# Performance work log

Measured on AMD Instinct MI355X. Metric: run time of the kernel, lower is better.

## Reference

```python
import jax, jax.numpy as jnp
import numpy as np

B, DIM, N = 64, 128, 4000
H = 4
DH = DIM // H          # 32
CL = 50                # clusters (hardcoded in module)
K = 9                  # knn_num
SCALOR = DH ** -0.5


def setup_inputs() -> dict:
    key = jax.random.key(0)
    ks = jax.random.split(key, 16)
    s = 0.05
    inp = {
        'x': jax.random.normal(ks[0], (B, DIM, N, 1), jnp.float32),
        # conv_group1 / conv_group2: InstanceNorm(no affine) -> BN(affine) -> ReLU -> 1x1 conv
        'wg1': jax.random.normal(ks[1], (CL, DIM), jnp.float32) * s,
        'bg1': jnp.zeros((CL,), jnp.float32),
        'g1_gamma': jnp.ones((DIM,), jnp.float32),
        'g1_beta': jnp.zeros((DIM,), jnp.float32),
        'wg2': jax.random.normal(ks[2], (CL, DIM), jnp.float32) * s,
        'bg2': jnp.zeros((CL,), jnp.float32),
        'g2_gamma': jnp.ones((DIM,), jnp.float32),
        'g2_beta': jnp.zeros((DIM,), jnp.float32),
        # per-head 1x1 convs (stacked over heads)
        'qkv_w': jax.random.normal(ks[3], (H, DH, DIM), jnp.float32) * s,
        'qkv_b': jnp.zeros((H, DH), jnp.float32),
        'qkv1_w': jax.random.normal(ks[4], (H, 3 * DH, DIM), jnp.float32) * s,
        'qkv1_b': jnp.zeros((H, 3 * DH), jnp.float32),
        # GCBlock convs: conv1 (1,3) stride (1,3): 2*DH->DH ; conv2 (1,3): DH->DH
        'gc1_w': jax.random.normal(ks[5], (H, DH, 2 * DH, 3), jnp.float32) * s,
        'gc1_b': jnp.zeros((H, DH), jnp.float32),
        'gc1_gamma': jnp.ones((H, DH), jnp.float32),
        'gc1_beta': jnp.zeros((H, DH), jnp.float32),
        'gc2_w': jax.random.normal(ks[6], (H, DH, DH, 3), jnp.float32) * s,
        'gc2_b': jnp.zeros((H, DH), jnp.float32),
        'gc2_gamma': jnp.ones((H, DH), jnp.float32),
        'gc2_beta': jnp.zeros((H, DH), jnp.float32),
        # output projections
        'pres_w': jax.random.normal(ks[7], (DIM, 2 * DIM), jnp.float32) * s,
        'pres_b': jnp.zeros((DIM,), jnp.float32),
        'proj_w': jax.random.normal(ks[8], (DIM, DIM), jnp.float32) * s,
        'proj_b': jnp.zeros((DIM,), jnp.float32),
    }
    return inp


def _conv_group(x3, w, bconv, gamma, beta):
    # x3: (b, C, n). InstanceNorm2d(eps=1e-3, no affine) over n, BN(train) over (b,n), ReLU, 1x1 conv.
    mu = x3.mean(-1, keepdims=True)
    var = x3.var(-1, keepdims=True)
    xin = (x3 - mu) * jax.lax.rsqrt(var + 1e-3)
    mu2 = xin.mean((0, 2), keepdims=True)
    var2 = xin.var((0, 2), keepdims=True)
    xbn = gamma[None, :, None] * (xin - mu2) * jax.lax.rsqrt(var2 + 1e-5) + beta[None, :, None]
    xr = jax.nn.relu(xbn)
    return jnp.einsum('oc,bcn->bon', w, xr) + bconv[None, :, None]


def _bn_train(h, gamma, beta, axes):
    mu = h.mean(axes, keepdims=True)
    var = h.var(axes, keepdims=True)
    return gamma * (h - mu) * jax.lax.rsqrt(var + 1e-5) + beta


def _forward(x, wg1, bg1, g1_gamma, g1_beta, wg2, bg2, g2_gamma, g2_beta,
             qkv_w, qkv_b, qkv1_w, qkv1_b,
             gc1_w, gc1_b, gc1_gamma, gc1_beta,
             gc2_w, gc2_b, gc2_gamma, gc2_beta,
             pres_w, pres_b, proj_w, proj_b):
    xs = x[..., 0]                                          # (b, dim, n)
    # cluster assignment 1: softmax over points
    embed1 = _conv_group(xs, wg1, bg1, g1_gamma, g1_beta)   # (b, 50, n)
    S1 = jax.nn.softmax(embed1, axis=2)
    cluster_x = jnp.einsum('bdn,bcn->bdc', xs, S1)          # (b, dim, 50)

    # ---- local branch (per head, vectorized): 1x1 conv -> knn graph feature -> conv stack ----
    q = jnp.einsum('hod,bdc->bhoc', qkv_w, cluster_x) + qkv_b[None, :, :, None]  # (b,H,dh,50)
    xt = q.transpose(0, 1, 3, 2)                            # (b,H,50,dh)
    inner = jnp.einsum('bhnc,bhmc->bhnm', xt, xt)
    sq = jnp.sum(xt * xt, axis=-1)
    pd = 2.0 * inner - sq[..., :, None] - sq[..., None, :]  # negative squared distance
    idx = jax.lax.top_k(pd, K)[1]                            # (b,H,50,K)
    x_exp = jnp.broadcast_to(xt[:, :, None, :, :], xt.shape[:2] + (CL, CL, DH))
    feature = jnp.take_along_axis(x_exp, idx[..., None], axis=3)        # (b,H,50,K,dh)
    center = jnp.broadcast_to(xt[:, :, :, None, :], feature.shape)
    edge = jnp.concatenate([center, center - feature], axis=-1)          # (b,H,50,K,2dh)
    # conv1: kernel (1,3) stride (1,3): K=9 -> 3 windows of 3
    e = edge.reshape(edge.shape[0], H, CL, 3, 3, 2 * DH)
    h1 = jnp.einsum('bhnjti,hoit->bhnjo', e, gc1_w) + gc1_b[None, :, None, None, :]
    h1 = jax.nn.relu(_bn_train(h1, gc1_gamma[None, :, None, None, :], gc1_beta[None, :, None, None, :], (0, 2, 3)))
    # conv2: kernel (1,3): 3 -> 1
    h2 = jnp.einsum('bhnti,hoit->bhno', h1, gc2_w) + gc2_b[None, :, None, :]
    h2 = jax.nn.relu(_bn_train(h2, gc2_gamma[None, :, None, :], gc2_beta[None, :, None, :], (0, 2)))
    local = h2.transpose(0, 1, 3, 2)                        # (b,H,dh,50)

    # ---- global branch: tiny attention over 50 clusters per head ----
    qkv = jnp.einsum('hod,bdc->bhoc', qkv1_w, cluster_x) + qkv1_b[None, :, :, None]  # (b,H,3dh,50)
    qg, kg, vg = jnp.split(qkv, 3, axis=2)
    attn = jax.nn.softmax(SCALOR * jnp.einsum('bhdn,bhdm->bhnm', qg, kg), axis=-1)
    glob = jnp.einsum('bhnm,bhdm->bhdn', attn, vg)          # (b,H,dh,50)

    # interleave [local_h, global_h] per head along channels -> (b, 2*dim, 50)
    per_head = jnp.concatenate([local, glob], axis=2)       # (b,H,2dh,50)
    cat = per_head.reshape(per_head.shape[0], 2 * DIM, CL)
    res = jnp.einsum('oc,bcn->bon', pres_w, cat) + pres_b[None, :, None]  # (b,dim,50)

    # cluster assignment 2: softmax over clusters, scatter back to points
    embed2 = _conv_group(xs, wg2, bg2, g2_gamma, g2_beta)   # (b,50,n)
    S2 = jax.nn.softmax(embed2, axis=1)
    res2 = jnp.einsum('bdc,bcn->bdn', res, S2)              # (b,dim,n)
    out = jnp.einsum('od,bdn->bon', proj_w, res2) + proj_b[None, :, None]
    return out[..., None]                                   # (b,dim,n,1)


def reference(x, wg1, bg1, g1_gamma, g1_beta, wg2, bg2, g2_gamma, g2_beta,
              qkv_w, qkv_b, qkv1_w, qkv1_b,
              gc1_w, gc1_b, gc1_gamma, gc1_beta,
              gc2_w, gc2_b, gc2_gamma, gc2_beta,
              pres_w, pres_b, proj_w, proj_b):
    return _forward(x, wg1, bg1, g1_gamma, g1_beta, wg2, bg2, g2_gamma, g2_beta,
                    qkv_w, qkv_b, qkv1_w, qkv1_b,
                    gc1_w, gc1_b, gc1_gamma, gc1_beta,
                    gc2_w, gc2_b, gc2_gamma, gc2_beta,
                    pres_w, pres_b, proj_w, proj_b)
```

## Files before the change

### kernel.cpp

```cpp
#include <hip/hip_runtime.h>
#include <cstddef>


constexpr size_t O_MU    = 0;
constexpr size_t O_RINV  = 8192;
constexpr size_t O_RATIO = 16384;
constexpr size_t O_A1    = 24576;
constexpr size_t O_B1    = 24704;
constexpr size_t O_A2    = 24832;
constexpr size_t O_B2    = 24960;
constexpr size_t O_PROJWT= 25088;
constexpr size_t O_VPROJ = 41472;
constexpr size_t O_MT    = 41600;
constexpr size_t O_E2    = 74368;
constexpr size_t O_UCXP  = 12874368;
constexpr size_t O_XT    = 17068672;
constexpr size_t O_QT    = 17478272;
constexpr size_t O_KT    = 17887872;
constexpr size_t O_VT    = 18297472;
constexpr size_t O_H1    = 18707072;
constexpr size_t O_P1    = 19935872;
constexpr size_t O_H2    = 19952512;
constexpr size_t O_P2    = 20362112;
constexpr size_t O_CAT   = 20378752;
constexpr size_t O_PRES2 = 21197952;

__global__ __launch_bounds__(256) void k_rowstats(const float* __restrict__ x,
                                                  float* __restrict__ ws){
  int w = threadIdx.x >> 6, lane = threadIdx.x & 63;
  int row = blockIdx.x*4 + w;
  const float4* xr = (const float4*)(x + (size_t)row * 4000);
  float s = 0.f, sq = 0.f;
  for(int i = lane; i < 1000; i += 64){
    float4 v = xr[i];
    s  += v.x + v.y + v.z + v.w;
    sq += v.x*v.x + v.y*v.y + v.z*v.z + v.w*v.w;
  }
  for(int off = 32; off > 0; off >>= 1){
    s  += __shfl_down(s,  off, 64);
    sq += __shfl_down(sq, off, 64);
  }
  if(lane == 0){
    float mean = s * (1.f/4000.f);
    float var  = sq * (1.f/4000.f) - mean*mean;
    ws[O_MU   + row] = mean;
    ws[O_RINV + row] = rsqrtf(var + 1e-3f);
    ws[O_RATIO+ row] = var / (var + 1e-3f);
  }
}

__global__ __launch_bounds__(256) void k_prep(const float* g1g, const float* g1b,
                       const float* g2g, const float* g2b,
                       const float* projw, float* __restrict__ ws){
  int t = threadIdx.x;
  int i = blockIdx.x*256 + t;
  { int o = i & 127, k = i >> 7; ws[O_PROJWT+i] = projw[o*128 + k]; }
  if(blockIdx.x == 0 && t < 128){
    float s = 0.f;
    for(int b = 0; b < 64; b++) s += ws[O_RATIO + b*128 + t];
    float var2 = s * (1.f/64.f);
    float inv2 = rsqrtf(var2 + 1e-5f);
    ws[O_A1+t] = g1g[t] * inv2;  ws[O_B1+t] = g1b[t];
    ws[O_A2+t] = g2g[t] * inv2;  ws[O_B2+t] = g2b[t];
  }
}

__global__ __launch_bounds__(256) void k_mprep(const float* __restrict__ presw,
                                               const float* __restrict__ presb,
                                               float* __restrict__ ws){
  int t = threadIdx.x;
  if(blockIdx.x < 128){
    int kk2 = blockIdx.x * 2;
    __shared__ float pwc[2][128];
    { int which = t >> 7, d = t & 127; pwc[which][d] = presw[d*256 + kk2 + which]; }
    __syncthreads();
    int which = t >> 7, o = t & 127;
    float acc = 0.f;
    for(int d = 0; d < 128; d++) acc += ws[O_PROJWT + d*128 + o] * pwc[which][d];
    ws[O_MT + (size_t)(kk2 + which)*128 + o] = acc;
  }else{
    if(t < 128){
      float v = 0.f;
      for(int d = 0; d < 128; d++) v += ws[O_PROJWT + d*128 + t] * presb[d];
      ws[O_VPROJ + t] = v;
    }
  }
}

__global__ __launch_bounds__(256) void k_e1ucx(const float* __restrict__ x,
    const float* __restrict__ wg1, const float* __restrict__ bg1,
    float* __restrict__ ws){
  int ch = blockIdx.x, b = blockIdx.y;
  __shared__ float lW1[128*52];
  __shared__ float lrv1[128*48];
  __shared__ float lxt [48*132];
  __shared__ float ca1[128], cb1[128];
  __shared__ float bg1p[56];
  int t = threadIdx.x;
  if(t < 128){
    float mu = ws[O_MU + b*128 + t], ri = ws[O_RINV + b*128 + t];
    float a1 = ws[O_A1+t]*ri;
    ca1[t] = a1; cb1[t] = ws[O_B1+t] - a1*mu;
  }
  if(t < 56) bg1p[t] = (t < 50) ? bg1[t] : 0.f;
  for(int i = t; i < 1664; i += 256){
    int cl = i >> 5, cq = i & 31;
    float4 w = (cl < 50) ? *(const float4*)&wg1[cl*128 + cq*4] : make_float4(0.f,0.f,0.f,0.f);
    int c0 = cq*4;
    lW1[(c0+0)*52+cl] = w.x; lW1[(c0+1)*52+cl] = w.y;
    lW1[(c0+2)*52+cl] = w.z; lW1[(c0+3)*52+cl] = w.w;
  }
  int dg = t & 31, cg = t >> 5;
  float ua[4][8];
  #pragma unroll
  for(int r = 0; r < 4; r++)
    #pragma unroll
    for(int i = 0; i < 8; i++) ua[r][i] = 0.f;
  float zacc = 0.f;
  int ig = t >> 4, jg = t & 15;
  int clb = ig*4, j4 = jg*4;
  int sc[6], sj[6];
  float4 pf[6];
  #pragma unroll
  for(int j = 0; j < 6; j++){ int i = t + 256*j; sc[j] = i/12; sj[j] = (i%12)*4; }
  #pragma unroll
  for(int j = 0; j < 6; j++)
    pf[j] = *(const float4*)&x[(size_t)(b*128 + sc[j])*4000 + ch*500 + sj[j]];

  for(int st = 0; st < 11; st++){
    int lim = (st == 10) ? 20 : 48;
    __syncthreads();
    #pragma unroll
    for(int j = 0; j < 6; j++){
      int c = sc[j], jj = sj[j];
      float4 xv = (jj < lim) ? pf[j] : make_float4(0.f,0.f,0.f,0.f);
      lxt[(jj+0)*132 + c] = xv.x; lxt[(jj+1)*132 + c] = xv.y;
      lxt[(jj+2)*132 + c] = xv.z; lxt[(jj+3)*132 + c] = xv.w;
      float a1 = ca1[c], b1v = cb1[c];
      float4 r1;
      r1.x = fmaxf(a1*xv.x + b1v, 0.f); r1.y = fmaxf(a1*xv.y + b1v, 0.f);
      r1.z = fmaxf(a1*xv.z + b1v, 0.f); r1.w = fmaxf(a1*xv.w + b1v, 0.f);
      *(float4*)&lrv1[c*48 + jj] = r1;
    }
    __syncthreads();
    if(st < 10){
      int lim2 = (st == 9) ? 20 : 48;
      int nb2 = ch*500 + (st+1)*48;
      #pragma unroll
      for(int j = 0; j < 6; j++)
        pf[j] = (sj[j] < lim2) ? *(const float4*)&x[(size_t)(b*128 + sc[j])*4000 + nb2 + sj[j]]
                               : make_float4(0.f,0.f,0.f,0.f);
    }
    float e[4][4];
    if(ig < 13 && jg < 12){
      #pragma unroll
      for(int r = 0; r < 4; r++){ e[r][0]=0.f; e[r][1]=0.f; e[r][2]=0.f; e[r][3]=0.f; }
      #pragma unroll 4
      for(int c = 0; c < 128; c++){
        float4 w = *(const float4*)&lW1[c*52 + clb];
        float4 v = *(const float4*)&lrv1[c*48 + j4];
        e[0][0] += w.x*v.x; e[0][1] += w.x*v.y; e[0][2] += w.x*v.z; e[0][3] += w.x*v.w;
        e[1][0] += w.y*v.x; e[1][1] += w.y*v.y; e[1][2] += w.y*v.z; e[1][3] += w.y*v.w;
        e[2][0] += w.z*v.x; e[2][1] += w.z*v.y; e[2][2] += w.z*v.z; e[2][3] += w.z*v.w;
        e[3][0] += w.w*v.x; e[3][1] += w.w*v.y; e[3][2] += w.w*v.z; e[3][3] += w.w*v.w;
      }
    }
    __syncthreads();
    if(ig < 13 && jg < 12){
      bool live = (j4 < lim);
      #pragma unroll
      for(int r = 0; r < 4; r++){
        float bias = bg1p[clb + r];
        float4 u = make_float4(0.f,0.f,0.f,0.f);
        if(live){
          u.x = expf(e[r][0] + bias); u.y = expf(e[r][1] + bias);
          u.z = expf(e[r][2] + bias); u.w = expf(e[r][3] + bias);
        }
        *(float4*)&lrv1[(clb + r)*48 + j4] = u;
      }
    }
    __syncthreads();
    if(t < 224){
      int d4 = dg*4, c8 = cg*8;
      for(int n4 = 0; n4 < 12; n4++){
        int n0 = n4*4;
        float4 uv[8];
        #pragma unroll
        for(int i = 0; i < 8; i++) uv[i] = *(const float4*)&lrv1[(c8 + i)*48 + n0];
        {
          float4 xq = *(const float4*)&lxt[(n0+0)*132 + d4];
          #pragma unroll
          for(int i = 0; i < 8; i++){
            float u = uv[i].x;
            ua[0][i] += xq.x*u; ua[1][i] += xq.y*u; ua[2][i] += xq.z*u; ua[3][i] += xq.w*u;
          }
        }
        {
          float4 xq = *(const float4*)&lxt[(n0+1)*132 + d4];
          #pragma unroll
          for(int i = 0; i < 8; i++){
            float u = uv[i].y;
            ua[0][i] += xq.x*u; ua[1][i] += xq.y*u; ua[2][i] += xq.z*u; ua[3][i] += xq.w*u;
          }
        }
        {
          float4 xq = *(const float4*)&lxt[(n0+2)*132 + d4];
          #pragma unroll
          for(int i = 0; i < 8; i++){
            float u = uv[i].z;
            ua[0][i] += xq.x*u; ua[1][i] += xq.y*u; ua[2][i] += xq.z*u; ua[3][i] += xq.w*u;
          }
        }
        {
          float4 xq = *(const float4*)&lxt[(n0+3)*132 + d4];
          #pragma unroll
          for(int i = 0; i < 8; i++){
            float u = uv[i].w;
            ua[0][i] += xq.x*u; ua[1][i] += xq.y*u; ua[2][i] += xq.z*u; ua[3][i] += xq.w*u;
          }
        }
      }
    }
    if(t < 52){
      float s = 0.f;
      #pragma unroll
      for(int k = 0; k < 12; k++){
        float4 u = *(const float4*)&lrv1[t*48 + k*4];
        s += u.x + u.y + u.z + u.w;
      }
      zacc += s;
    }
  }
  if(t < 224){
    int d4 = dg*4, c8 = cg*8;
    #pragma unroll
    for(int r = 0; r < 4; r++){
      size_t base = O_UCXP + ((size_t)(ch*64 + b)*132 + d4 + r)*56 + c8;
      *(float4*)&ws[base]     = make_float4(ua[r][0], ua[r][1], ua[r][2], ua[r][3]);
      *(float4*)&ws[base + 4] = make_float4(ua[r][4], ua[r][5], ua[r][6], ua[r][7]);
    }
  }
  if(t < 52) ws[O_UCXP + ((size_t)(ch*64 + b)*132 + 128)*56 + t] = zacc;
}

__global__ __launch_bounds__(256) void k_e2(const float* __restrict__ x,
    const float* __restrict__ wg2, const float* __restrict__ bg2,
    float* __restrict__ ws){
  int ch = blockIdx.x, b = blockIdx.y;
  __shared__ float lW2[128*52];
  __shared__ float lrv2[128*48];
  __shared__ float ca2[128], cb2[128];
  __shared__ float bg2p[56];
  int t = threadIdx.x;
  if(t < 128){
    float mu = ws[O_MU + b*128 + t], ri = ws[O_RINV + b*128 + t];
    float a2 = ws[O_A2+t]*ri;
    ca2[t] = a2; cb2[t] = ws[O_B2+t] - a2*mu;
  }
  if(t < 56) bg2p[t] = (t < 50) ? bg2[t] : 0.f;
  for(int i = t; i < 1664; i += 256){
    int cl = i >> 5, cq = i & 31;
    float4 w = (cl < 50) ? *(const float4*)&wg2[cl*128 + cq*4] : make_float4(0.f,0.f,0.f,0.f);
    int c0 = cq*4;
    lW2[(c0+0)*52+cl] = w.x; lW2[(c0+1)*52+cl] = w.y;
    lW2[(c0+2)*52+cl] = w.z; lW2[(c0+3)*52+cl] = w.w;
  }
  int ig = t >> 4, jg = t & 15;
  int clb = ig*4, j4 = jg*4;
  int sc[6], sj[6];
  float4 pf[6];
  #pragma unroll
  for(int j = 0; j < 6; j++){ int i = t + 256*j; sc[j] = i/12; sj[j] = (i%12)*4; }
  #pragma unroll
  for(int j = 0; j < 6; j++)
    pf[j] = *(const float4*)&x[(size_t)(b*128 + sc[j])*4000 + ch*500 + sj[j]];

  for(int st = 0; st < 11; st++){
    int nb = ch*500 + st*48;
    int lim = (st == 10) ? 20 : 48;
    __syncthreads();
    #pragma unroll
    for(int j = 0; j < 6; j++){
      int c = sc[j], jj = sj[j];
      float4 xv = (jj < lim) ? pf[j] : make_float4(0.f,0.f,0.f,0.f);
      float a2 = ca2[c], b2v = cb2[c];
      float4 r2;
      r2.x = fmaxf(a2*xv.x + b2v, 0.f); r2.y = fmaxf(a2*xv.y + b2v, 0.f);
      r2.z = fmaxf(a2*xv.z + b2v, 0.f); r2.w = fmaxf(a2*xv.w + b2v, 0.f);
      *(float4*)&lrv2[c*48 + jj] = r2;
    }
    __syncthreads();
    if(st < 10){
      int lim2 = (st == 9) ? 20 : 48;
      int nb2 = ch*500 + (st+1)*48;
      #pragma unroll
      for(int j = 0; j < 6; j++)
        pf[j] = (sj[j] < lim2) ? *(const float4*)&x[(size_t)(b*128 + sc[j])*4000 + nb2 + sj[j]]
                               : make_float4(0.f,0.f,0.f,0.f);
    }
    if(ig < 13 && jg < 12){
      float e[4][4];
      #pragma unroll
      for(int r = 0; r < 4; r++){ e[r][0]=0.f; e[r][1]=0.f; e[r][2]=0.f; e[r][3]=0.f; }
      #pragma unroll 4
      for(int c = 0; c < 128; c++){
        float4 w = *(const float4*)&lW2[c*52 + clb];
        float4 v = *(const float4*)&lrv2[c*48 + j4];
        e[0][0] += w.x*v.x; e[0][1] += w.x*v.y; e[0][2] += w.x*v.z; e[0][3] += w.x*v.w;
        e[1][0] += w.y*v.x; e[1][1] += w.y*v.y; e[1][2] += w.y*v.z; e[1][3] += w.y*v.w;
        e[2][0] += w.z*v.x; e[2][1] += w.z*v.y; e[2][2] += w.z*v.z; e[2][3] += w.z*v.w;
        e[3][0] += w.w*v.x; e[3][1] += w.w*v.y; e[3][2] += w.w*v.z; e[3][3] += w.w*v.w;
      }
      if(j4 < lim){
        #pragma unroll
        for(int r = 0; r < 4; r++){
          int cl = clb + r;
          if(cl < 50){
            float bias = bg2p[cl];
            float4 o = make_float4(e[r][0]+bias, e[r][1]+bias, e[r][2]+bias, e[r][3]+bias);
            *(float4*)&ws[O_E2 + ((size_t)b*50 + cl)*4000 + nb + j4] = o;
          }
        }
      }
    }
  }
}

__global__ __launch_bounds__(256) void k_qkv(const float* __restrict__ qw,
                                             const float* __restrict__ qb,
                                             const float* __restrict__ q1w,
                                             const float* __restrict__ q1b,
                                             float* __restrict__ ws){
  int rt = blockIdx.x, b = blockIdx.y;
  __shared__ float wl[64*130];
  __shared__ float cxl[128*52];
  __shared__ float zi[52];
  int t = threadIdx.x;
  if(t < 52){
    float s = 0.f;
    if(t < 50){
      #pragma unroll
      for(int ch = 0; ch < 8; ch++)
        s += ws[O_UCXP + ((size_t)(ch*64 + b)*132 + 128)*56 + t];
      zi[t] = 1.f / s;
    }else zi[t] = 0.f;
  }
  for(int i = t; i < 2048; i += 256){
    int rl = i >> 5, kq = i & 31, row = rt*64 + rl;
    float4 w = (row < 128) ? *(const float4*)&qw[row*128 + kq*4]
                           : *(const float4*)&q1w[(row-128)*128 + kq*4];
    int k0 = kq*4;
    wl[rl*130 + k0+0] = w.x; wl[rl*130 + k0+1] = w.y;
    wl[rl*130 + k0+2] = w.z; wl[rl*130 + k0+3] = w.w;
  }
  __syncthreads();
  for(int i = t; i < 6656; i += 256){
    int k = i / 52, c = i % 52;
    float s = 0.f;
    size_t base = O_UCXP + ((size_t)b*132 + k)*56 + c;
    #pragma unroll
    for(int ch = 0; ch < 8; ch++) s += ws[base + (size_t)ch*64*132*56];
    cxl[i] = s * zi[c];
  }
  __syncthreads();
  int ig = t & 15, cg = t >> 4;
  float acc[4][4];
  #pragma unroll
  for(int r = 0; r < 4; r++){ acc[r][0]=0.f; acc[r][1]=0.f; acc[r][2]=0.f; acc[r][3]=0.f; }
// ... 24 lines not shown
      }
      #pragma unroll
      for(int s = 0; s < 4; s++){
        int c = cg*4 + s;
        if(c < 50) ws[base + (size_t)c*32] = acc[r][s] + bias;
      }
    }
  }
}

__global__ __launch_bounds__(256) void k_knn(const float* __restrict__ g1w,
                                             const float* __restrict__ g1bias,
                                             float* __restrict__ ws){
  int h = blockIdx.x, b = blockIdx.y;
  __shared__ float xtl[50][33];
  __shared__ float pdl[50][52];
  __shared__ float sql[50];
  __shared__ int   idxl[50][9];
  __shared__ float w1l[6144];
  int t = threadIdx.x;
  const float* xtg = ws + O_XT + (size_t)(b*4 + h)*1600;
  for(int i = t; i < 1600; i += 256) xtl[i >> 5][i & 31] = xtg[i];
  for(int i = t; i < 6144; i += 256){
    int o = i / 192, r = i % 192, ii = r / 3, tt = r % 3;
    w1l[(ii*3 + tt)*32 + o] = g1w[(size_t)h*6144 + i];
  }
  __syncthreads();
  if(t < 50){
    float s = 0.f;
    for(int d = 0; d < 32; d++){ float v = xtl[t][d]; s += v*v; }
    sql[t] = s;
  }
  __syncthreads();
  for(int i = t; i < 2500; i += 256){
    int n = i / 50, m = i % 50;
    float s = 0.f;
    for(int d = 0; d < 32; d++) s += xtl[n][d]*xtl[m][d];
    pdl[n][m] = 2.f*s - sql[n] - sql[m];
  }
  __syncthreads();
  if(t < 50){
    float pv = INFINITY; int pi = -1;
    for(int k = 0; k < 9; k++){
      float bv = -INFINITY; int bi = 1000;
      for(int m = 0; m < 50; m++){
        float v = pdl[t][m];
        bool elig = (v < pv) || (v == pv && m > pi);
        if(elig && (v > bv || (v == bv && m < bi))){ bv = v; bi = m; }
      }
      idxl[t][k] = bi; pv = bv; pi = bi;
    }
  }
  __syncthreads();
  if(t < 150){
    int n = t / 3, jw = t % 3;
    float acc[32];
    #pragma unroll
    for(int o = 0; o < 32; o++) acc[o] = 0.f;
    for(int t3 = 0; t3 < 3; t3++){
      int kx = idxl[n][jw*3 + t3];
      for(int ii = 0; ii < 32; ii++){
        float c0 = xtl[n][ii];
        float c1 = c0 - xtl[kx][ii];
        const float* wr0 = w1l + (ii*3 + t3)*32;
        const float* wr1 = w1l + ((ii+32)*3 + t3)*32;
        #pragma unroll
        for(int o = 0; o < 32; o++) acc[o] += c0*wr0[o] + c1*wr1[o];
      }
    }
    float* out = ws + O_H1 + ((size_t)(b*4 + h)*150 + n*3 + jw)*32;
    #pragma unroll
    for(int o = 0; o < 32; o++) out[o] = acc[o] + g1bias[h*32 + o];
  }
}

__global__ __launch_bounds__(256) void k_bn1p(float* __restrict__ ws){
  int h = blockIdx.x, b = blockIdx.y, t = threadIdx.x;
  int o = t & 31, part = t >> 5;
  const float* src = ws + O_H1 + (size_t)(b*4 + h)*4800;
  float s = 0.f, sq = 0.f;
  for(int nj = part; nj < 150; nj += 8){
    float v = src[nj*32 + o];
    s += v; sq += v*v;
  }
  __shared__ float rs[8][33], rq[8][33];
  rs[part][o] = s; rq[part][o] = sq; __syncthreads();
  if(t < 32){
    float S = 0.f, Q = 0.f;
    for(int p = 0; p < 8; p++){ S += rs[p][t]; Q += rq[p][t]; }
    ws[O_P1 + b*256 + h*32 + t]       = S;
    ws[O_P1 + b*256 + 128 + h*32 + t] = Q;
  }
}

__global__ __launch_bounds__(256) void k_conv2(const float* __restrict__ g1g,
                                               const float* __restrict__ g1be,
                                               const float* __restrict__ g2w,
                                               const float* __restrict__ g2bias,
                                               float* __restrict__ ws){
  int h = blockIdx.x, b = blockIdx.y;
  __shared__ float hl[150][33];
  __shared__ float w2l[3072];
  __shared__ float rs[8][32], rq[8][32];
  __shared__ float b1s[32], b1t[32];
  int t = threadIdx.x;
  if(t < 32){
    float s = 0.f, sq = 0.f;
    for(int bb = 0; bb < 64; bb++){
      s  += ws[O_P1 + bb*256 + h*32 + t];
      sq += ws[O_P1 + bb*256 + 128 + h*32 + t];
    }
    float mean = s * (1.f/9600.f), var = sq * (1.f/9600.f) - mean*mean;
    float sc = g1g[h*32+t] * rsqrtf(var + 1e-5f);
    b1s[t] = sc; b1t[t] = g1be[h*32+t] - sc*mean;
  }
  for(int i = t; i < 3072; i += 256){
    int o = i / 96, r = i % 96, ii = r / 3, tt = r % 3;
    w2l[(ii*3 + tt)*32 + o] = g2w[(size_t)h*3072 + i];
  }
  __syncthreads();
  const float* h1p = ws + O_H1 + (size_t)(b*4 + h)*4800;
  for(int i = t; i < 4800; i += 256){
    int nj = i >> 5, ii = i & 31;
    hl[nj][ii] = fmaxf(b1s[ii]*h1p[i] + b1t[ii], 0.f);
  }
  __syncthreads();
  int o = t & 31, ng = t >> 5;
  float bias = g2bias[h*32 + o];
  float s = 0.f, sq = 0.f;
  for(int n = ng; n < 50; n += 8){
    float acc = 0.f;
    for(int t3 = 0; t3 < 3; t3++){
      const float* hr = hl[n*3 + t3];
      #pragma unroll
      for(int ii = 0; ii < 32; ii++) acc += hr[ii] * w2l[(ii*3 + t3)*32 + o];
    }
    acc += bias;
    ws[O_H2 + ((size_t)(b*4 + h)*50 + n)*32 + o] = acc;
    s += acc; sq += acc*acc;
  }
  rs[ng][o] = s; rq[ng][o] = sq; __syncthreads();
  if(t < 32){
    float S = 0.f, Q = 0.f;
    for(int g2 = 0; g2 < 8; g2++){ S += rs[g2][t]; Q += rq[g2][t]; }
// ... 4 lines not shown

__global__ __launch_bounds__(256) void k_attn(const float* __restrict__ g2g,
                                              const float* __restrict__ g2be,
                                              float* __restrict__ ws){
  int h = blockIdx.x, b = blockIdx.y;
  __shared__ float qtl[50][33], ktl[50][33], vtl[50][33], al[50][52];
  __shared__ float b2s[32], b2t[32];
  int t = threadIdx.x;
  if(t < 32){
    float s = 0.f, sq = 0.f;
    for(int bb = 0; bb < 64; bb++){
      s  += ws[O_P2 + (size_t)(bb*4 + h)*64 + t];
      sq += ws[O_P2 + (size_t)(bb*4 + h)*64 + 32 + t];
    }
    float mean = s * (1.f/3200.f), var = sq * (1.f/3200.f) - mean*mean;
    float sc = g2g[h*32+t] * rsqrtf(var + 1e-5f);
    b2s[t] = sc; b2t[t] = g2be[h*32+t] - sc*mean;
  }
  size_t base = (size_t)(b*4 + h)*1600;
  for(int i = t; i < 1600; i += 256){
    int n = i >> 5, d = i & 31;
    qtl[n][d] = ws[O_QT + base + i];
    ktl[n][d] = ws[O_KT + base + i];
    vtl[n][d] = ws[O_VT + base + i];
  }
  __syncthreads();
  for(int i = t; i < 2500; i += 256){
    int n = i / 50, m = i % 50;
    float s = 0.f;
    for(int d = 0; d < 32; d++) s += qtl[n][d]*ktl[m][d];
    al[n][m] = s * 0.17677669529663687f;
  }
  __syncthreads();
  if(t < 50){
    float m = -INFINITY;
    for(int j = 0; j < 50; j++) m = fmaxf(m, al[t][j]);
    float s = 0.f;
    for(int j = 0; j < 50; j++){ float e = expf(al[t][j] - m); al[t][j] = e; s += e; }
    float inv = 1.f/s;
    for(int j = 0; j < 50; j++) al[t][j] *= inv;
  }
  __syncthreads();
  for(int i = t; i < 1600; i += 256){
    int n = i >> 5, d = i & 31;
    float gacc = 0.f;
    for(int m = 0; m < 50; m++) gacc += al[n][m]*vtl[m][d];
    ws[O_CAT + ((size_t)b*256 + h*64 + 32 + d)*50 + n] = gacc;
    float l = fmaxf(b2s[d]*ws[O_H2 + ((size_t)(b*4 + h)*50 + n)*32 + d] + b2t[d], 0.f);
    ws[O_CAT + ((size_t)b*256 + h*64 + d)*50 + n] = l;
  }
}

__global__ __launch_bounds__(256) void k_res(float* __restrict__ ws){
  int b = blockIdx.x;
  __shared__ float mtl[64*132];
  __shared__ float catl[64*52];
  __shared__ float vp[128];
  int t = threadIdx.x;
  if(t < 128) vp[t] = ws[O_VPROJ + t];
  int og = t >> 4, cg = t & 15;
  int ob = og*8, cb = cg*4;
  float acc[8][4];
  #pragma unroll
  for(int r = 0; r < 8; r++){ acc[r][0]=0.f; acc[r][1]=0.f; acc[r][2]=0.f; acc[r][3]=0.f; }
  for(int kc = 0; kc < 4; kc++){
    int k0 = kc*64;
    __syncthreads();
    for(int i = t; i < 2048; i += 256){
      int k = i >> 5, oq = i & 31;
      float4 m = *(const float4*)&ws[O_MT + (size_t)(k0 + k)*128 + oq*4];
      *(float4*)&mtl[k*132 + oq*4] = m;
    }
    for(int i = t; i < 3328; i += 256){
      int k = i / 52, c = i % 52;
      catl[i] = (c < 50) ? ws[O_CAT + (size_t)b*12800 + (k0 + k)*50 + c] : 0.f;
    }
    __syncthreads();
    if(cg < 13){
      #pragma unroll 2
      for(int k = 0; k < 64; k++){
        float4 m0 = *(const float4*)&mtl[k*132 + ob];
        float4 m1 = *(const float4*)&mtl[k*132 + ob + 4];
        float4 cv = *(const float4*)&catl[k*52 + cb];
        acc[0][0] += m0.x*cv.x; acc[0][1] += m0.x*cv.y; acc[0][2] += m0.x*cv.z; acc[0][3] += m0.x*cv.w;
        acc[1][0] += m0.y*cv.x; acc[1][1] += m0.y*cv.y; acc[1][2] += m0.y*cv.z; acc[1][3] += m0.y*cv.w;
        acc[2][0] += m0.z*cv.x; acc[2][1] += m0.z*cv.y; acc[2][2] += m0.z*cv.z; acc[2][3] += m0.z*cv.w;
        acc[3][0] += m0.w*cv.x; acc[3][1] += m0.w*cv.y; acc[3][2] += m0.w*cv.z; acc[3][3] += m0.w*cv.w;
        acc[4][0] += m1.x*cv.x; acc[4][1] += m1.x*cv.y; acc[4][2] += m1.x*cv.z; acc[4][3] += m1.x*cv.w;
        acc[5][0] += m1.y*cv.x; acc[5][1] += m1.y*cv.y; acc[5][2] += m1.y*cv.z; acc[5][3] += m1.y*cv.w;
        acc[6][0] += m1.z*cv.x; acc[6][1] += m1.z*cv.y; acc[6][2] += m1.z*cv.z; acc[6][3] += m1.z*cv.w;
        acc[7][0] += m1.w*cv.x; acc[7][1] += m1.w*cv.y; acc[7][2] += m1.w*cv.z; acc[7][3] += m1.w*cv.w;
      }
    }
  }
  if(cg < 13){
    #pragma unroll
    for(int s = 0; s < 4; s++){
      int c = cb + s;
      if(c < 50){
        float4 o0 = make_float4(acc[0][s]+vp[ob+0], acc[1][s]+vp[ob+1], acc[2][s]+vp[ob+2], acc[3][s]+vp[ob+3]);
        float4 o1 = make_float4(acc[4][s]+vp[ob+4], acc[5][s]+vp[ob+5], acc[6][s]+vp[ob+6], acc[7][s]+vp[ob+7]);
        *(float4*)&ws[O_PRES2 + (size_t)b*6400 + c*128 + ob]     = o0;
        *(float4*)&ws[O_PRES2 + (size_t)b*6400 + c*128 + ob + 4] = o1;
      }
    }
  }
}

__global__ __launch_bounds__(256) void k_out(const float* __restrict__ projb,
                                             float* __restrict__ ws,
                                             float* __restrict__ out){
  int nt = blockIdx.x, b = blockIdx.y;
  int n0 = nt*64;
  __shared__ float sl[50*64];
  __shared__ float p2l[50*132];
  __shared__ float pb[128];
  int t = threadIdx.x;
  for(int i = t; i < 3200; i += 256){
    int c = i >> 6, j = i & 63, n = n0 + j;
    sl[i] = (n < 4000) ? ws[O_E2 + ((size_t)b*50 + c)*4000 + n] : 0.f;
  }
  for(int i = t; i < 6400; i += 256){
    int c = i >> 7, o = i & 127;
    p2l[c*132 + o] = ws[O_PRES2 + (size_t)b*6400 + c*128 + o];
  }
  if(t < 128) pb[t] = projb[t];
  __syncthreads();
  if(t < 64){
    int j = t;
    float m = -INFINITY;
    for(int c = 0; c < 50; c++) m = fmaxf(m, sl[c*64 + j]);
    float s = 0.f;
    for(int c = 0; c < 50; c++){ float e = expf(sl[c*64 + j] - m); sl[c*64 + j] = e; s += e; }
    float inv = 1.f/s;
    for(int c = 0; c < 50; c++) sl[c*64 + j] *= inv;
  }
  __syncthreads();
  int og = t >> 4, jg = t & 15;
  int ob = og*8, j4 = jg*4;
  float acc[8][4];
  #pragma unroll
  for(int r = 0; r < 8; r++){ acc[r][0]=0.f; acc[r][1]=0.f; acc[r][2]=0.f; acc[r][3]=0.f; }
  #pragma unroll 2
  for(int c = 0; c < 50; c++){
    float4 sv = *(const float4*)&sl[c*64 + j4];
    float4 p0 = *(const float4*)&p2l[c*132 + ob];
    float4 p1 = *(const float4*)&p2l[c*132 + ob + 4];
    acc[0][0] += p0.x*sv.x; acc[0][1] += p0.x*sv.y; acc[0][2] += p0.x*sv.z; acc[0][3] += p0.x*sv.w;
    acc[1][0] += p0.y*sv.x; acc[1][1] += p0.y*sv.y; acc[1][2] += p0.y*sv.z; acc[1][3] += p0.y*sv.w;
    acc[2][0] += p0.z*sv.x; acc[2][1] += p0.z*sv.y; acc[2][2] += p0.z*sv.z; acc[2][3] += p0.z*sv.w;
    acc[3][0] += p0.w*sv.x; acc[3][1] += p0.w*sv.y; acc[3][2] += p0.w*sv.z; acc[3][3] += p0.w*sv.w;
    acc[4][0] += p1.x*sv.x; acc[4][1] += p1.x*sv.y; acc[4][2] += p1.x*sv.z; acc[4][3] += p1.x*sv.w;
    acc[5][0] += p1.y*sv.x; acc[5][1] += p1.y*sv.y; acc[5][2] += p1.y*sv.z; acc[5][3] += p1.y*sv.w;
    acc[6][0] += p1.z*sv.x; acc[6][1] += p1.z*sv.y; acc[6][2] += p1.z*sv.z; acc[6][3] += p1.z*sv.w;
    acc[7][0] += p1.w*sv.x; acc[7][1] += p1.w*sv.y; acc[7][2] += p1.w*sv.z; acc[7][3] += p1.w*sv.w;
  }
  int n = n0 + j4;
  if(n < 4000){
    #pragma unroll
    for(int r = 0; r < 8; r++){
      float bv = pb[ob + r];
      float4 o = make_float4(acc[r][0]+bv, acc[r][1]+bv, acc[r][2]+bv, acc[r][3]+bv);
      *(float4*)&out[(size_t)(b*128 + ob + r)*4000 + n] = o;
    }
  }
}

extern "C" void kernel_launch(void* const* d_in, const int* in_sizes, int n_in,
                              void* d_out, int out_size, void* d_ws, size_t ws_size,
                              hipStream_t stream){
  (void)in_sizes; (void)n_in; (void)out_size; (void)ws_size;
  const float* x      = (const float*)d_in[0];
  const float* wg1    = (const float*)d_in[1];
  const float* bg1    = (const float*)d_in[2];
  const float* g1g    = (const float*)d_in[3];
  const float* g1b    = (const float*)d_in[4];
  const float* wg2    = (const float*)d_in[5];
  const float* bg2    = (const float*)d_in[6];
  const float* g2g    = (const float*)d_in[7];
  const float* g2b    = (const float*)d_in[8];
  const float* qkvw   = (const float*)d_in[9];
  const float* qkvb   = (const float*)d_in[10];
  const float* qkv1w  = (const float*)d_in[11];
  const float* qkv1b  = (const float*)d_in[12];
  const float* gc1w   = (const float*)d_in[13];
  const float* gc1bias= (const float*)d_in[14];
  const float* gc1g   = (const float*)d_in[15];
  const float* gc1be  = (const float*)d_in[16];
  const float* gc2w   = (const float*)d_in[17];
  const float* gc2bias= (const float*)d_in[18];
  const float* gc2g   = (const float*)d_in[19];
  const float* gc2be  = (const float*)d_in[20];
  const float* presw  = (const float*)d_in[21];
  const float* presb  = (const float*)d_in[22];
  const float* projw  = (const float*)d_in[23];
  const float* projb  = (const float*)d_in[24];
  float* ws = (float*)d_ws;
  float* out = (float*)d_out;

  k_rowstats<<<2048, 256, 0, stream>>>(x, ws);
  k_prep<<<64, 256, 0, stream>>>(g1g, g1b, g2g, g2b, projw, ws);
  k_mprep<<<129, 256, 0, stream>>>(presw, presb, ws);
  k_e1ucx<<<dim3(8, 64), 256, 0, stream>>>(x, wg1, bg1, ws);
  k_e2<<<dim3(8, 64), 256, 0, stream>>>(x, wg2, bg2, ws);
  k_qkv<<<dim3(8, 64), 256, 0, stream>>>(qkvw, qkvb, qkv1w, qkv1b, ws);
  k_knn<<<dim3(4, 64), 256, 0, stream>>>(gc1w, gc1bias, ws);
  k_bn1p<<<dim3(4, 64), 256, 0, stream>>>(ws);
  k_conv2<<<dim3(4, 64), 256, 0, stream>>>(gc1g, gc1be, gc2w, gc2bias, ws);
  k_attn<<<dim3(4, 64), 256, 0, stream>>>(gc2g, gc2be, ws);
  k_res<<<64, 256, 0, stream>>>(ws);
  k_out<<<dim3(63, 64), 256, 0, stream>>>(projb, ws, out);
}
```

Before: 779.3 us.

## Merge small kernels, double block size in e1/e2, split k_res work

Folds the prep work into the stats and mprep kernels and folds the BN1 partial sums into the knn kernel, cutting three launches. k_e1ucx and k_e2 move to 512-thread blocks with smaller per-thread tiles, and k_e2 uses a finer grid (12 chunks of 336 points). The lxt shared buffer gets an XOR swizzle in place of padding. k_res is split across two blocks per batch by output half so more CUs are used. The cost is more synchronisation per block and a heavier knn kernel, in exchange for more parallelism and fewer launches.

```diff
diff --git a/kernel.cpp b/kernel.cpp
--- a/kernel.cpp
+++ b/kernel.cpp
@@ -25,8 +25,15 @@
 constexpr size_t O_CAT   = 20378752;
 constexpr size_t O_PRES2 = 21197952;
 
-__global__ __launch_bounds__(256) void k_rowstats(const float* __restrict__ x,
-                                                  float* __restrict__ ws){
+__global__ __launch_bounds__(256) void k_stats(const float* __restrict__ x,
+                                               const float* __restrict__ projw,
+                                               float* __restrict__ ws){
+  if(blockIdx.x >= 2048){
+    int i = (blockIdx.x - 2048)*256 + threadIdx.x;
+    int o = i & 127, k = i >> 7;
+    ws[O_PROJWT + i] = projw[o*128 + k];
+    return;
+  }
   int w = threadIdx.x >> 6, lane = threadIdx.x & 63;
   int row = blockIdx.x*4 + w;
   const float4* xr = (const float4*)(x + (size_t)row * 4000);
@@ -49,24 +56,12 @@
   }
 }
 
-__global__ __launch_bounds__(256) void k_prep(const float* g1g, const float* g1b,
-                       const float* g2g, const float* g2b,
-                       const float* projw, float* __restrict__ ws){
-  int t = threadIdx.x;
-  int i = blockIdx.x*256 + t;
-  { int o = i & 127, k = i >> 7; ws[O_PROJWT+i] = projw[o*128 + k]; }
-  if(blockIdx.x == 0 && t < 128){
-    float s = 0.f;
-    for(int b = 0; b < 64; b++) s += ws[O_RATIO + b*128 + t];
-    float var2 = s * (1.f/64.f);
-    float inv2 = rsqrtf(var2 + 1e-5f);
-    ws[O_A1+t] = g1g[t] * inv2;  ws[O_B1+t] = g1b[t];
-    ws[O_A2+t] = g2g[t] * inv2;  ws[O_B2+t] = g2b[t];
-  }
-}
-
 __global__ __launch_bounds__(256) void k_mprep(const float* __restrict__ presw,
                                                const float* __restrict__ presb,
+                                               const float* __restrict__ g1g,
+                                               const float* __restrict__ g1b,
+                                               const float* __restrict__ g2g,
+                                               const float* __restrict__ g2b,
                                                float* __restrict__ ws){
   int t = threadIdx.x;
   if(blockIdx.x < 128){
@@ -78,22 +73,31 @@
     float acc = 0.f;
     for(int d = 0; d < 128; d++) acc += ws[O_PROJWT + d*128 + o] * pwc[which][d];
     ws[O_MT + (size_t)(kk2 + which)*128 + o] = acc;
-  }else{
+  }else if(blockIdx.x == 128){
     if(t < 128){
       float v = 0.f;
       for(int d = 0; d < 128; d++) v += ws[O_PROJWT + d*128 + t] * presb[d];
       ws[O_VPROJ + t] = v;
     }
-  }
-}
-
-__global__ __launch_bounds__(256) void k_e1ucx(const float* __restrict__ x,
+  }else{
+    if(t < 128){
+      float s = 0.f;
+      for(int b = 0; b < 64; b++) s += ws[O_RATIO + b*128 + t];
+      float var2 = s * (1.f/64.f);
+      float inv2 = rsqrtf(var2 + 1e-5f);
+      ws[O_A1+t] = g1g[t] * inv2;  ws[O_B1+t] = g1b[t];
+      ws[O_A2+t] = g2g[t] * inv2;  ws[O_B2+t] = g2b[t];
+    }
+  }
+}
+
+__global__ __launch_bounds__(512, 4) void k_e1ucx(const float* __restrict__ x,
     const float* __restrict__ wg1, const float* __restrict__ bg1,
     float* __restrict__ ws){
   int ch = blockIdx.x, b = blockIdx.y;
   __shared__ float lW1[128*52];
   __shared__ float lrv1[128*48];
-  __shared__ float lxt [48*132];
+  __shared__ float lxt [48*128];
   __shared__ float ca1[128], cb1[128];
   __shared__ float bg1p[56];
   int t = threadIdx.x;
@@ -102,8 +106,8 @@
     float a1 = ws[O_A1+t]*ri;
     ca1[t] = a1; cb1[t] = ws[O_B1+t] - a1*mu;
   }
-  if(t < 56) bg1p[t] = (t < 50) ? bg1[t] : 0.f;
-  for(int i = t; i < 1664; i += 256){
+  if(t >= 448 && t < 504){ int q = t - 448; bg1p[q] = (q < 50) ? bg1[q] : 0.f; }
+  for(int i = t; i < 1664; i += 512){
     int cl = i >> 5, cq = i & 31;
     float4 w = (cl < 50) ? *(const float4*)&wg1[cl*128 + cq*4] : make_float4(0.f,0.f,0.f,0.f);
     int c0 = cq*4;
@@ -111,31 +115,34 @@
     lW1[(c0+2)*52+cl] = w.z; lW1[(c0+3)*52+cl] = w.w;
   }
   int dg = t & 31, cg = t >> 5;
-  float ua[4][8];
+  int d4 = dg*4, c4 = cg*4;
+  float ua[4][4];
   #pragma unroll
-  for(int r = 0; r < 4; r++)
-    #pragma unroll
-    for(int i = 0; i < 8; i++) ua[r][i] = 0.f;
+  for(int r = 0; r < 4; r++){ ua[r][0]=0.f; ua[r][1]=0.f; ua[r][2]=0.f; ua[r][3]=0.f; }
   float zacc = 0.f;
   int ig = t >> 4, jg = t & 15;
-  int clb = ig*4, j4 = jg*4;
-  int sc[6], sj[6];
-  float4 pf[6];
+  int clb = ig*2, j4 = jg*4;
+  int sc[3], sj[3], cx[3];
+  float4 pf[3];
   #pragma unroll
-  for(int j = 0; j < 6; j++){ int i = t + 256*j; sc[j] = i/12; sj[j] = (i%12)*4; }
+  for(int j = 0; j < 3; j++){
+    int i = t + 512*j;
+    sc[j] = i/12; sj[j] = (i%12)*4;
+    cx[j] = sc[j] ^ (((sj[j] >> 2) & 7) << 2);
+  }
   #pragma unroll
-  for(int j = 0; j < 6; j++)
+  for(int j = 0; j < 3; j++)
     pf[j] = *(const float4*)&x[(size_t)(b*128 + sc[j])*4000 + ch*500 + sj[j]];
 
   for(int st = 0; st < 11; st++){
     int lim = (st == 10) ? 20 : 48;
     __syncthreads();
     #pragma unroll
-    for(int j = 0; j < 6; j++){
-      int c = sc[j], jj = sj[j];
+    for(int j = 0; j < 3; j++){
+      int c = sc[j], jj = sj[j], cxx = cx[j];
       float4 xv = (jj < lim) ? pf[j] : make_float4(0.f,0.f,0.f,0.f);
-      lxt[(jj+0)*132 + c] = xv.x; lxt[(jj+1)*132 + c] = xv.y;
-      lxt[(jj+2)*132 + c] = xv.z; lxt[(jj+3)*132 + c] = xv.w;
+      lxt[(jj+0)*128 + cxx] = xv.x; lxt[(jj+1)*128 + cxx] = xv.y;
+      lxt[(jj+2)*128 + cxx] = xv.z; lxt[(jj+3)*128 + cxx] = xv.w;
       float a1 = ca1[c], b1v = cb1[c];
       float4 r1;
       r1.x = fmaxf(a1*xv.x + b1v, 0.f); r1.y = fmaxf(a1*xv.y + b1v, 0.f);
@@ -147,29 +154,27 @@
       int lim2 = (st == 9) ? 20 : 48;
       int nb2 = ch*500 + (st+1)*48;
       #pragma unroll
-      for(int j = 0; j < 6; j++)
+      for(int j = 0; j < 3; j++)
         pf[j] = (sj[j] < lim2) ? *(const float4*)&x[(size_t)(b*128 + sc[j])*4000 + nb2 + sj[j]]
                                : make_float4(0.f,0.f,0.f,0.f);
     }
-    float e[4][4];
-    if(ig < 13 && jg < 12){
-      #pragma unroll
-      for(int r = 0; r < 4; r++){ e[r][0]=0.f; e[r][1]=0.f; e[r][2]=0.f; e[r][3]=0.f; }
+    float e[2][4];
+    if(ig < 26 && jg < 12){
+      e[0][0]=0.f; e[0][1]=0.f; e[0][2]=0.f; e[0][3]=0.f;
+      e[1][0]=0.f; e[1][1]=0.f; e[1][2]=0.f; e[1][3]=0.f;
       #pragma unroll 4
       for(int c = 0; c < 128; c++){
-        float4 w = *(const float4*)&lW1[c*52 + clb];
+        float2 w = *(const float2*)&lW1[c*52 + clb];
         float4 v = *(const float4*)&lrv1[c*48 + j4];
         e[0][0] += w.x*v.x; e[0][1] += w.x*v.y; e[0][2] += w.x*v.z; e[0][3] += w.x*v.w;
         e[1][0] += w.y*v.x; e[1][1] += w.y*v.y; e[1][2] += w.y*v.z; e[1][3] += w.y*v.w;
-        e[2][0] += w.z*v.x; e[2][1] += w.z*v.y; e[2][2] += w.z*v.z; e[2][3] += w.z*v.w;
-        e[3][0] += w.w*v.x; e[3][1] += w.w*v.y; e[3][2] += w.w*v.z; e[3][3] += w.w*v.w;
-      }
-    }
-    __syncthreads();
-    if(ig < 13 && jg < 12){
+      }
+    }
+    __syncthreads();
+    if(ig < 26 && jg < 12){
       bool live = (j4 < lim);
       #pragma unroll
-      for(int r = 0; r < 4; r++){
+      for(int r = 0; r < 2; r++){
         float bias = bg1p[clb + r];
         float4 u = make_float4(0.f,0.f,0.f,0.f);
         if(live){
@@ -180,45 +185,26 @@
       }
     }
     __syncthreads();
-    if(t < 224){
-      int d4 = dg*4, c8 = cg*8;
+    if(cg < 14){
+      #pragma unroll 2
       for(int n4 = 0; n4 < 12; n4++){
         int n0 = n4*4;
-        float4 uv[8];
-        #pragma unroll
-        for(int i = 0; i < 8; i++) uv[i] = *(const float4*)&lrv1[(c8 + i)*48 + n0];
-        {
-          float4 xq = *(const float4*)&lxt[(n0+0)*132 + d4];
-          #pragma unroll
-          for(int i = 0; i < 8; i++){
-            float u = uv[i].x;
-            ua[0][i] += xq.x*u; ua[1][i] += xq.y*u; ua[2][i] += xq.z*u; ua[3][i] += xq.w*u;
-          }
-        }
-        {
-          float4 xq = *(const float4*)&lxt[(n0+1)*132 + d4];
-          #pragma unroll
-          for(int i = 0; i < 8; i++){
-            float u = uv[i].y;
-            ua[0][i] += xq.x*u; ua[1][i] += xq.y*u; ua[2][i] += xq.z*u; ua[3][i] += xq.w*u;
-          }
-        }
-        {
-          float4 xq = *(const float4*)&lxt[(n0+2)*132 + d4];
-          #pragma unroll
-          for(int i = 0; i < 8; i++){
-            float u = uv[i].z;
-            ua[0][i] += xq.x*u; ua[1][i] += xq.y*u; ua[2][i] += xq.z*u; ua[3][i] += xq.w*u;
-          }
-        }
-        {
-          float4 xq = *(const float4*)&lxt[(n0+3)*132 + d4];
-          #pragma unroll
-          for(int i = 0; i < 8; i++){
-            float u = uv[i].w;
-            ua[0][i] += xq.x*u; ua[1][i] += xq.y*u; ua[2][i] += xq.z*u; ua[3][i] += xq.w*u;
-          }
-        }
+        int dx = d4 ^ ((n4 & 7) << 2);
+        float4 u0 = *(const float4*)&lrv1[(c4+0)*48 + n0];
+        float4 u1 = *(const float4*)&lrv1[(c4+1)*48 + n0];
+        float4 u2 = *(const float4*)&lrv1[(c4+2)*48 + n0];
+        float4 u3 = *(const float4*)&lrv1[(c4+3)*48 + n0];
+        float4 x0 = *(const float4*)&lxt[(n0+0)*128 + dx];
+        float4 x1 = *(const float4*)&lxt[(n0+1)*128 + dx];
+        float4 x2 = *(const float4*)&lxt[(n0+2)*128 + dx];
+        float4 x3 = *(const float4*)&lxt[(n0+3)*128 + dx];
+        #define ACC4(r, XC) \
+          ua[r][0] += x0.XC*u0.x + x1.XC*u0.y + x2.XC*u0.z + x3.XC*u0.w; \
+          ua[r][1] += x0.XC*u1.x + x1.XC*u1.y + x2.XC*u1.z + x3.XC*u1.w; \
+          ua[r][2] += x0.XC*u2.x + x1.XC*u2.y + x2.XC*u2.z + x3.XC*u2.w; \
+          ua[r][3] += x0.XC*u3.x + x1.XC*u3.y + x2.XC*u3.z + x3.XC*u3.w;
+        ACC4(0, x) ACC4(1, y) ACC4(2, z) ACC4(3, w)
+        #undef ACC4
       }
     }
     if(t < 52){
@@ -231,19 +217,17 @@
       zacc += s;
     }
   }
-  if(t < 224){
-    int d4 = dg*4, c8 = cg*8;
+  if(cg < 14){
     #pragma unroll
     for(int r = 0; r < 4; r++){
-      size_t base = O_UCXP + ((size_t)(ch*64 + b)*132 + d4 + r)*56 + c8;
-      *(float4*)&ws[base]     = make_float4(ua[r][0], ua[r][1], ua[r][2], ua[r][3]);
-      *(float4*)&ws[base + 4] = make_float4(ua[r][4], ua[r][5], ua[r][6], ua[r][7]);
+      size_t base = O_UCXP + ((size_t)(ch*64 + b)*132 + d4 + r)*56 + c4;
+      *(float4*)&ws[base] = make_float4(ua[r][0], ua[r][1], ua[r][2], ua[r][3]);
     }
   }
   if(t < 52) ws[O_UCXP + ((size_t)(ch*64 + b)*132 + 128)*56 + t] = zacc;
 }
 
-__global__ __launch_bounds__(256) void k_e2(const float* __restrict__ x,
+__global__ __launch_bounds__(512, 6) void k_e2(const float* __restrict__ x,
     const float* __restrict__ wg2, const float* __restrict__ bg2,
     float* __restrict__ ws){
   int ch = blockIdx.x, b = blockIdx.y;
@@ -257,8 +241,8 @@
     float a2 = ws[O_A2+t]*ri;
     ca2[t] = a2; cb2[t] = ws[O_B2+t] - a2*mu;
   }
-  if(t < 56) bg2p[t] = (t < 50) ? bg2[t] : 0.f;
-  for(int i = t; i < 1664; i += 256){
+  if(t >= 448 && t < 504){ int q = t - 448; bg2p[q] = (q < 50) ? bg2[q] : 0.f; }
+  for(int i = t; i < 1664; i += 512){
     int cl = i >> 5, cq = i & 31;
     float4 w = (cl < 50) ? *(const float4*)&wg2[cl*128 + cq*4] : make_float4(0.f,0.f,0.f,0.f);
     int c0 = cq*4;
@@ -266,21 +250,25 @@
     lW2[(c0+2)*52+cl] = w.z; lW2[(c0+3)*52+cl] = w.w;
   }
   int ig = t >> 4, jg = t & 15;
-  int clb = ig*4, j4 = jg*4;
-  int sc[6], sj[6];
-  float4 pf[6];
+  int clb = ig*2, j4 = jg*4;
+  int sc[3], sj[3];
+  float4 pf[3];
   #pragma unroll
-  for(int j = 0; j < 6; j++){ int i = t + 256*j; sc[j] = i/12; sj[j] = (i%12)*4; }
-  #pragma unroll
-  for(int j = 0; j < 6; j++)
-    pf[j] = *(const float4*)&x[(size_t)(b*128 + sc[j])*4000 + ch*500 + sj[j]];
-
-  for(int st = 0; st < 11; st++){
-    int nb = ch*500 + st*48;
-    int lim = (st == 10) ? 20 : 48;
-    __syncthreads();
-    #pragma unroll
-    for(int j = 0; j < 6; j++){
+  for(int j = 0; j < 3; j++){ int i = t + 512*j; sc[j] = i/12; sj[j] = (i%12)*4; }
+  {
+    int nb0 = ch*336;
+    int lim0 = 4000 - nb0; if(lim0 > 48) lim0 = 48;
+    #pragma unroll
+    for(int j = 0; j < 3; j++)
+      pf[j] = (sj[j] < lim0) ? *(const float4*)&x[(size_t)(b*128 + sc[j])*4000 + nb0 + sj[j]]
+                             : make_float4(0.f,0.f,0.f,0.f);
+  }
+  for(int st = 0; st < 7; st++){
+    int nb = ch*336 + st*48;
+    int lim = 4000 - nb; if(lim > 48) lim = 48;
+    __syncthreads();
+    #pragma unroll
+    for(int j = 0; j < 3; j++){
       int c = sc[j], jj = sj[j];
       float4 xv = (jj < lim) ? pf[j] : make_float4(0.f,0.f,0.f,0.f);
       float a2 = ca2[c], b2v = cb2[c];
@@ -290,30 +278,28 @@
       *(float4*)&lrv2[c*48 + jj] = r2;
     }
     __syncthreads();
-    if(st < 10){
-      int lim2 = (st == 9) ? 20 : 48;
-      int nb2 = ch*500 + (st+1)*48;
+    if(st < 6){
+      int nb2 = nb + 48;
+      int lim2 = 4000 - nb2; if(lim2 > 48) lim2 = 48;
       #pragma unroll
-      for(int j = 0; j < 6; j++)
+      for(int j = 0; j < 3; j++)
         pf[j] = (sj[j] < lim2) ? *(const float4*)&x[(size_t)(b*128 + sc[j])*4000 + nb2 + sj[j]]
                                : make_float4(0.f,0.f,0.f,0.f);
     }
-    if(ig < 13 && jg < 12){
-      float e[4][4];
-      #pragma unroll
-      for(int r = 0; r < 4; r++){ e[r][0]=0.f; e[r][1]=0.f; e[r][2]=0.f; e[r][3]=0.f; }
+    if(ig < 26 && jg < 12){
+      float e[2][4];
+      e[0][0]=0.f; e[0][1]=0.f; e[0][2]=0.f; e[0][3]=0.f;
+      e[1][0]=0.f; e[1][1]=0.f; e[1][2]=0.f; e[1][3]=0.f;
       #pragma unroll 4
       for(int c = 0; c < 128; c++){
-        float4 w = *(const float4*)&lW2[c*52 + clb];
+        float2 w = *(const float2*)&lW2[c*52 + clb];
         float4 v = *(const float4*)&lrv2[c*48 + j4];
         e[0][0] += w.x*v.x; e[0][1] += w.x*v.y; e[0][2] += w.x*v.z; e[0][3] += w.x*v.w;
         e[1][0] += w.y*v.x; e[1][1] += w.y*v.y; e[1][2] += w.y*v.z; e[1][3] += w.y*v.w;
-        e[2][0] += w.z*v.x; e[2][1] += w.z*v.y; e[2][2] += w.z*v.z; e[2][3] += w.z*v.w;
-        e[3][0] += w.w*v.x; e[3][1] += w.w*v.y; e[3][2] += w.w*v.z; e[3][3] += w.w*v.w;
       }
       if(j4 < lim){
         #pragma unroll
-        for(int r = 0; r < 4; r++){
+        for(int r = 0; r < 2; r++){
           int cl = clb + r;
           if(cl < 50){
             float bias = bg2p[cl];
@@ -444,9 +430,10 @@
     }
   }
   __syncthreads();
-  if(t < 150){
+  float acc[32];
+  bool act = (t < 150);
+  if(act){
     int n = t / 3, jw = t % 3;
-    float acc[32];
     #pragma unroll
     for(int o = 0; o < 32; o++) acc[o] = 0.f;
     for(int t3 = 0; t3 < 3; t3++){
@@ -462,26 +449,30 @@
     }
     float* out = ws + O_H1 + ((size_t)(b*4 + h)*150 + n*3 + jw)*32;
     #pragma unroll
-    for(int o = 0; o < 32; o++) out[o] = acc[o] + g1bias[h*32 + o];
-  }
-}
-
-__global__ __launch_bounds__(256) void k_bn1p(float* __restrict__ ws){
-  int h = blockIdx.x, b = blockIdx.y, t = threadIdx.x;
-  int o = t & 31, part = t >> 5;
-  const float* src = ws + O_H1 + (size_t)(b*4 + h)*4800;
-  float s = 0.f, sq = 0.f;
-  for(int nj = part; nj < 150; nj += 8){
-    float v = src[nj*32 + o];
-    s += v; sq += v*v;
-  }
-  __shared__ float rs[8][33], rq[8][33];
-  rs[part][o] = s; rq[part][o] = sq; __syncthreads();
-  if(t < 32){
-    float S = 0.f, Q = 0.f;
-    for(int p = 0; p < 8; p++){ S += rs[p][t]; Q += rq[p][t]; }
-    ws[O_P1 + b*256 + h*32 + t]       = S;
-    ws[O_P1 + b*256 + 128 + h*32 + t] = Q;
+    for(int o = 0; o < 32; o++){ acc[o] += g1bias[h*32 + o]; out[o] = acc[o]; }
+  }
+  __syncthreads();
+  if(act){
+    #pragma unroll
+    for(int o = 0; o < 32; o++) w1l[t*32 + o] = acc[o];
+  }
+  __syncthreads();
+  {
+    int o = t & 31, part = t >> 5;
+    float s = 0.f, sq = 0.f;
+    for(int r = part; r < 150; r += 8){
+      float v = w1l[r*32 + o];
+      s += v; sq += v*v;
+    }
+    float* sp = &pdl[0][0];
+    sp[part*32 + o] = s; sp[256 + part*32 + o] = sq;
+    __syncthreads();
+    if(t < 32){
+      float S = 0.f, Q = 0.f;
+      for(int p = 0; p < 8; p++){ S += sp[p*32 + t]; Q += sp[256 + p*32 + t]; }
+      ws[O_P1 + b*256 + h*32 + t]       = S;
+      ws[O_P1 + b*256 + 128 + h*32 + t] = Q;
+    }
   }
 }
 
@@ -592,24 +583,24 @@
 }
 
 __global__ __launch_bounds__(256) void k_res(float* __restrict__ ws){
-  int b = blockIdx.x;
-  __shared__ float mtl[64*132];
+  int oh = blockIdx.x & 1, b = blockIdx.x >> 1;
+  __shared__ float mtl[64*68];
   __shared__ float catl[64*52];
-  __shared__ float vp[128];
-  int t = threadIdx.x;
-  if(t < 128) vp[t] = ws[O_VPROJ + t];
+  __shared__ float vp[64];
+  int t = threadIdx.x;
+  if(t < 64) vp[t] = ws[O_VPROJ + oh*64 + t];
   int og = t >> 4, cg = t & 15;
-  int ob = og*8, cb = cg*4;
-  float acc[8][4];
+  int ob = og*4, cb = cg*4;
+  float acc[4][4];
   #pragma unroll
-  for(int r = 0; r < 8; r++){ acc[r][0]=0.f; acc[r][1]=0.f; acc[r][2]=0.f; acc[r][3]=0.f; }
+  for(int r = 0; r < 4; r++){ acc[r][0]=0.f; acc[r][1]=0.f; acc[r][2]=0.f; acc[r][3]=0.f; }
   for(int kc = 0; kc < 4; kc++){
     int k0 = kc*64;
     __syncthreads();
-    for(int i = t; i < 2048; i += 256){
-      int k = i >> 5, oq = i & 31;
-      float4 m = *(const float4*)&ws[O_MT + (size_t)(k0 + k)*128 + oq*4];
-      *(float4*)&mtl[k*132 + oq*4] = m;
+    for(int i = t; i < 1024; i += 256){
+      int k = i >> 4, oq = i & 15;
+      float4 m = *(const float4*)&ws[O_MT + (size_t)(k0 + k)*128 + oh*64 + oq*4];
+      *(float4*)&mtl[k*68 + oq*4] = m;
     }
     for(int i = t; i < 3328; i += 256){
       int k = i / 52, c = i % 52;
@@ -619,17 +610,12 @@
     if(cg < 13){
       #pragma unroll 2
       for(int k = 0; k < 64; k++){
-        float4 m0 = *(const float4*)&mtl[k*132 + ob];
-        float4 m1 = *(const float4*)&mtl[k*132 + ob + 4];
+        float4 m0 = *(const float4*)&mtl[k*68 + ob];
         float4 cv = *(const float4*)&catl[k*52 + cb];
         acc[0][0] += m0.x*cv.x; acc[0][1] += m0.x*cv.y; acc[0][2] += m0.x*cv.z; acc[0][3] += m0.x*cv.w;
         acc[1][0] += m0.y*cv.x; acc[1][1] += m0.y*cv.y; acc[1][2] += m0.y*cv.z; acc[1][3] += m0.y*cv.w;
         acc[2][0] += m0.z*cv.x; acc[2][1] += m0.z*cv.y; acc[2][2] += m0.z*cv.z; acc[2][3] += m0.z*cv.w;
         acc[3][0] += m0.w*cv.x; acc[3][1] += m0.w*cv.y; acc[3][2] += m0.w*cv.z; acc[3][3] += m0.w*cv.w;
-        acc[4][0] += m1.x*cv.x; acc[4][1] += m1.x*cv.y; acc[4][2] += m1.x*cv.z; acc[4][3] += m1.x*cv.w;
-        acc[5][0] += m1.y*cv.x; acc[5][1] += m1.y*cv.y; acc[5][2] += m1.y*cv.z; acc[5][3] += m1.y*cv.w;
-        acc[6][0] += m1.z*cv.x; acc[6][1] += m1.z*cv.y; acc[6][2] += m1.z*cv.z; acc[6][3] += m1.z*cv.w;
-        acc[7][0] += m1.w*cv.x; acc[7][1] += m1.w*cv.y; acc[7][2] += m1.w*cv.z; acc[7][3] += m1.w*cv.w;
       }
     }
   }
@@ -639,9 +625,7 @@
       int c = cb + s;
       if(c < 50){
         float4 o0 = make_float4(acc[0][s]+vp[ob+0], acc[1][s]+vp[ob+1], acc[2][s]+vp[ob+2], acc[3][s]+vp[ob+3]);
-        float4 o1 = make_float4(acc[4][s]+vp[ob+4], acc[5][s]+vp[ob+5], acc[6][s]+vp[ob+6], acc[7][s]+vp[ob+7]);
-        *(float4*)&ws[O_PRES2 + (size_t)b*6400 + c*128 + ob]     = o0;
-        *(float4*)&ws[O_PRES2 + (size_t)b*6400 + c*128 + ob + 4] = o1;
+        *(float4*)&ws[O_PRES2 + (size_t)b*6400 + c*128 + oh*64 + ob] = o0;
       }
     }
   }
@@ -738,16 +722,14 @@
   float* ws = (float*)d_ws;
   float* out = (float*)d_out;
 
-  k_rowstats<<<2048, 256, 0, stream>>>(x, ws);
-  k_prep<<<64, 256, 0, stream>>>(g1g, g1b, g2g, g2b, projw, ws);
-  k_mprep<<<129, 256, 0, stream>>>(presw, presb, ws);
-  k_e1ucx<<<dim3(8, 64), 256, 0, stream>>>(x, wg1, bg1, ws);
-  k_e2<<<dim3(8, 64), 256, 0, stream>>>(x, wg2, bg2, ws);
+  k_stats<<<2112, 256, 0, stream>>>(x, projw, ws);
+  k_mprep<<<130, 256, 0, stream>>>(presw, presb, g1g, g1b, g2g, g2b, ws);
+  k_e1ucx<<<dim3(8, 64), 512, 0, stream>>>(x, wg1, bg1, ws);
+  k_e2<<<dim3(12, 64), 512, 0, stream>>>(x, wg2, bg2, ws);
   k_qkv<<<dim3(8, 64), 256, 0, stream>>>(qkvw, qkvb, qkv1w, qkv1b, ws);
   k_knn<<<dim3(4, 64), 256, 0, stream>>>(gc1w, gc1bias, ws);
-  k_bn1p<<<dim3(4, 64), 256, 0, stream>>>(ws);
   k_conv2<<<dim3(4, 64), 256, 0, stream>>>(gc1g, gc1be, gc2w, gc2bias, ws);
   k_attn<<<dim3(4, 64), 256, 0, stream>>>(gc2g, gc2be, ws);
-  k_res<<<64, 256, 0, stream>>>(ws);
+  k_res<<<128, 256, 0, stream>>>(ws);
   k_out<<<dim3(63, 64), 256, 0, stream>>>(projb, ws, out);
 }
```

Result: no change. 787.6 us (+1.1%).
